# Kernel tuning notes

Hardware: AMD Instinct MI355X
Metric: run time of the kernel (lower is better)

Reference implementation:

```python
import jax, jax.numpy as jnp
import numpy as np

SDF_W = 7000.0
EIK_W = 600.0
ORI_W = 500.0
NEAR_ORI_W = 10.0
GRADN_W = 200.0
K_NEIGHBORS = 2


def _orientation_sign(query, surface, normals, k=K_NEIGHBORS):
    # Original detaches to numpy for a scipy KDTree query -> stop_gradient here.
    q = jax.lax.stop_gradient(query)       # [Q,3]
    s = jax.lax.stop_gradient(surface)     # [S,3]
    n = jax.lax.stop_gradient(normals)     # [S,3]
    # Brute-force squared distances [Q,S] (GEMM-dominated).
    d2 = (jnp.sum(q * q, axis=-1, keepdims=True)
          - 2.0 * (q @ s.T)
          + jnp.sum(s * s, axis=-1)[None, :])
    _, idx = jax.lax.top_k(-d2, k)         # [Q,k] nearest-neighbor indices
    near_pts = s[idx]                      # [Q,k,3]
    near_nrm = n[idx]                      # [Q,k,3]
    vecs = q[:, None, :] - near_pts        # [Q,k,3]
    dots = jnp.sum(vecs * near_nrm, axis=-1)  # [Q,k]
    return jnp.sign(jnp.mean(dots, axis=1))   # [Q]


def setup_inputs() -> dict:
    key = jax.random.key(0)
    ks = jax.random.split(key, 8)
    N = 16384
    return {
        "manifold_pred": jax.random.normal(ks[0], (N, 1), jnp.float32) * 0.1,
        "manifold_grad": jax.random.normal(ks[1], (N, 3), jnp.float32),
        "nonmanifold_pred": jax.random.normal(ks[2], (N, 1), jnp.float32),
        "near_points_pred": jax.random.normal(ks[3], (N, 1), jnp.float32) * 0.1,
        "surface_points": jax.random.normal(ks[4], (N, 3), jnp.float32),
        "surface_normals": jax.random.normal(ks[5], (N, 3), jnp.float32),
        "off_surface_points": jax.random.normal(ks[6], (N, 3), jnp.float32) * 1.5,
        "near_points": jax.random.normal(ks[7], (N, 3), jnp.float32),
    }


def reference(manifold_pred, manifold_grad, nonmanifold_pred, near_points_pred,
              surface_points, surface_normals, off_surface_points, near_points):
    sdf_loss = jnp.mean(manifold_pred ** 2)
    eikonal_loss = jnp.mean((jnp.linalg.norm(manifold_grad, axis=-1) - 1.0) ** 2)

    signs_off = _orientation_sign(off_surface_points, surface_points, surface_normals)
    orientation_loss = jnp.mean(jax.nn.relu(-nonmanifold_pred * signs_off[:, None]))

    signs_near = _orientation_sign(near_points, surface_points, surface_normals)
    near_surface_orientation_loss = jnp.mean(jax.nn.relu(-near_points_pred * signs_near[:, None]))

    gradient_normal_loss = jnp.mean((manifold_grad - surface_normals) ** 2)

    total = (SDF_W * sdf_loss + EIK_W * eikonal_loss + ORI_W * orientation_loss
             + NEAR_ORI_W * near_surface_orientation_loss + GRADN_W * gradient_normal_loss)
    return (total, sdf_loss, eikonal_loss, orientation_loss,
            near_surface_orientation_loss, gradient_normal_loss)
```

## Files before the change

kernel.cpp:

```cpp
#include <hip/hip_runtime.h>
#include <math.h>

#define SDF_W      7000.0f
#define EIK_W      600.0f
#define ORI_W      500.0f
#define NEAR_ORI_W 10.0f
#define GRADN_W    200.0f

#define TILE   2048
#define NWAVE  8
#define QPL    8
#define CHK    64
#define WS_STRIDE 512
#define WS_REC 4096

typedef float v2f __attribute__((ext_vector_type(2)));


__device__ __forceinline__ float nh2(float sx, float sy, float sz) {
    return -0.5f * fmaf(sx, sx, fmaf(sy, sy, sz * sz));
}
__device__ __forceinline__ float score(float qx, float qy, float qz,
                                       float sx, float sy, float sz, float nh) {
    return fmaf(qx, sx, fmaf(qy, sy, fmaf(qz, sz, nh)));
}

__global__ __launch_bounds__(512, 4) void nn_scan(
    const float* __restrict__ offq, const float* __restrict__ nearq,
    const float* __restrict__ surf,
    float* __restrict__ ws, int S, int Qoff, int QT, int splits, int segLen)
{
    __shared__ float4 tile[TILE];
    const int t    = threadIdx.x;
    const int lane = t & 63;
    const int wv   = __builtin_amdgcn_readfirstlane(t >> 6);

    const int qg = blockIdx.x / splits;
    const int sp = blockIdx.x % splits;
    const int sb = sp * segLen;
    int se = sb + segLen; if (se > S) se = S;

    float qx[QPL], qy[QPL], qz[QPL];
    #pragma unroll
    for (int k = 0; k < QPL; ++k) {
        int q = qg * 512 + k * 64 + lane;
        float x = 0.f, y = 0.f, z = 0.f;
        if (q < QT) {
            const float* p = (q < Qoff) ? (offq + 3 * q) : (nearq + 3 * (q - Qoff));
            x = p[0]; y = p[1]; z = p[2];
        }
        qx[k] = x; qy[k] = y; qz[k] = z;
    }
    v2f qx2[QPL/2], qy2[QPL/2], qz2[QPL/2];
    #pragma unroll
    for (int p = 0; p < QPL/2; ++p) {
        qx2[p] = (v2f){qx[2*p], qx[2*p+1]};
        qy2[p] = (v2f){qy[2*p], qy[2*p+1]};
        qz2[p] = (v2f){qz[2*p], qz[2*p+1]};
    }

    float M1[QPL], M2[QPL], P1[QPL], P2[QPL];
    int   c1[QPL], c2[QPL];
    const int cinit = (sb < S ? sb : 0) >> 6;
    #pragma unroll
    for (int k = 0; k < QPL; ++k) {
        M1[k] = -3.0e38f; M2[k] = -3.0e38f;
        P1[k] = -3.0e38f; P2[k] = -3.0e38f;
        c1[k] = cinit;    c2[k] = cinit;
    }

    for (int base = sb; base < se; base += TILE) {
        __syncthreads();
        #pragma unroll
        for (int k = 0; k < TILE / 512; ++k) {
            int li = k * 512 + t;
            int p  = base + li;
            float sx = 0.f, sy = 0.f, sz = 0.f, w = -3.0e38f;
            if (p < se) {
                sx = surf[3*p]; sy = surf[3*p+1]; sz = surf[3*p+2];
                w  = nh2(sx, sy, sz);
            }
            tile[li] = make_float4(sx, sy, sz, w);
        }
        __syncthreads();
        const int lo = wv * (TILE / NWAVE);
        const float4* tp = tile + lo;
        const int cidbase = (base + lo) >> 6;
        #pragma unroll 1
        for (int c = 0; c < (TILE / NWAVE) / CHK; ++c) {
            const float4* cp = tp + c * CHK;
            #pragma unroll 8
            for (int o = 0; o < CHK; ++o) {
                float4 s4 = cp[o];
                v2f sx = (v2f){s4.x, s4.x};
                v2f sy = (v2f){s4.y, s4.y};
                v2f sz = (v2f){s4.z, s4.z};
                v2f sw = (v2f){s4.w, s4.w};
                #pragma unroll
                for (int p = 0; p < QPL/2; ++p) {
                    v2f g = __builtin_elementwise_fma(qx2[p], sx,
                            __builtin_elementwise_fma(qy2[p], sy,
                            __builtin_elementwise_fma(qz2[p], sz, sw)));
                    float ga = g[0], gb = g[1];
                    M2[2*p]   = __builtin_amdgcn_fmed3f(ga, M1[2*p], M2[2*p]);
                    M1[2*p]   = fmaxf(M1[2*p], ga);
                    M2[2*p+1] = __builtin_amdgcn_fmed3f(gb, M1[2*p+1], M2[2*p+1]);
                    M1[2*p+1] = fmaxf(M1[2*p+1], gb);
                }
            }
            const int cid = cidbase + c;
            #pragma unroll
            for (int k = 0; k < QPL; ++k) {
                c1[k] = (M1[k] != P1[k]) ? cid : c1[k];  P1[k] = M1[k];
                c2[k] = (M2[k] != P2[k]) ? cid : c2[k];  P2[k] = M2[k];
            }
        }
    }

    float4* rec = tile;
    __syncthreads();
    if (wv >= 4) {
        #pragma unroll
        for (int k = 0; k < QPL; ++k)
            rec[(wv - 4) * 512 + k * 64 + lane] =
                make_float4(M1[k], M2[k], __int_as_float(c1[k]), __int_as_float(c2[k]));
    }
    __syncthreads();
    if (wv < 4) {
        #pragma unroll
        for (int k = 0; k < QPL; ++k) {
            float4 a = rec[wv * 512 + k * 64 + lane];
            float a1 = a.x, a2 = a.y;
            int ac1 = __float_as_int(a.z), ac2 = __float_as_int(a.w);
            if (a1 > M1[k])      { M2[k] = M1[k]; c2[k] = c1[k]; M1[k] = a1; c1[k] = ac1; }
            else if (a1 > M2[k]) { M2[k] = a1; c2[k] = ac1; }
            if (a2 > M2[k])      { M2[k] = a2; c2[k] = ac2; }
        }
    }
    __syncthreads();
    if (wv == 2 || wv == 3) {
        #pragma unroll
        for (int k = 0; k < QPL; ++k)
            rec[(wv - 2) * 512 + k * 64 + lane] =
                make_float4(M1[k], M2[k], __int_as_float(c1[k]), __int_as_float(c2[k]));
    }
    __syncthreads();
    if (wv < 2) {
        #pragma unroll
        for (int k = 0; k < QPL; ++k) {
            float4 a = rec[wv * 512 + k * 64 + lane];
            float a1 = a.x, a2 = a.y;
            int ac1 = __float_as_int(a.z), ac2 = __float_as_int(a.w);
            if (a1 > M1[k])      { M2[k] = M1[k]; c2[k] = c1[k]; M1[k] = a1; c1[k] = ac1; }
            else if (a1 > M2[k]) { M2[k] = a1; c2[k] = ac1; }
            if (a2 > M2[k])      { M2[k] = a2; c2[k] = ac2; }
        }
    }
    __syncthreads();
    if (wv == 1) {
        #pragma unroll
        for (int k = 0; k < QPL; ++k)
            rec[k * 64 + lane] =
                make_float4(M1[k], M2[k], __int_as_float(c1[k]), __int_as_float(c2[k]));
    }
    __syncthreads();
    if (wv == 0) {
        #pragma unroll
        for (int k = 0; k < QPL; ++k) {
            float4 a = rec[k * 64 + lane];
            float a1 = a.x, a2 = a.y;
            int ac1 = __float_as_int(a.z), ac2 = __float_as_int(a.w);
            if (a1 > M1[k])      { M2[k] = M1[k]; c2[k] = c1[k]; M1[k] = a1; c1[k] = ac1; }
            else if (a1 > M2[k]) { M2[k] = a1; c2[k] = ac1; }
            if (a2 > M2[k])      { M2[k] = a2; c2[k] = ac2; }
            int gq = qg * 512 + k * 64 + lane;
            if (gq < QT)
                ((float4*)(ws + WS_REC))[(size_t)gq * splits + sp] =
                    make_float4(M1[k], M2[k], __int_as_float(c1[k]), __int_as_float(c2[k]));
        }
    }
}

__global__ __launch_bounds__(256) void recover_k(
    const float* __restrict__ offq, const float* __restrict__ nearq,
    const float* __restrict__ surf, const float* __restrict__ norms,
    const float* __restrict__ nmpred, const float* __restrict__ nppred,
    const float* __restrict__ mp, const float* __restrict__ mg,
    const float* __restrict__ sn,
    float* __restrict__ ws, int S, int Qoff, int QT, int N, int splits)
{
    const int t    = threadIdx.x;
    const int lane = t & 63;
    const int wv   = t >> 6;
    const int gw   = blockIdx.x * 4 + wv;
    const int NW   = gridDim.x * 4;

    float ori = 0.f, nori = 0.f;
    for (int q = gw; q < QT; q += NW) {
        const float4* recs = ((const float4*)(ws + WS_REC)) + (size_t)q * splits;
        float4 r = recs[0];
        float M1 = r.x, M2 = r.y;
        int C1 = __float_as_int(r.z), C2 = __float_as_int(r.w);
        for (int i = 1; i < splits; ++i) {
            float4 a = recs[i];
            float a1 = a.x, a2 = a.y;
            int ac1 = __float_as_int(a.z), ac2 = __float_as_int(a.w);
            if (a1 > M1)      { M2 = M1; C2 = C1; M1 = a1; C1 = ac1; }
            else if (a1 > M2) { M2 = a1; C2 = ac1; }
            if (a2 > M2)      { M2 = a2; C2 = ac2; }
        }
        const bool isNear = (q >= Qoff);
        const float* qp = isNear ? (nearq + 3 * (q - Qoff)) : (offq + 3 * q);
        const float qx = qp[0], qy = qp[1], qz = qp[2];

        int j1 = C1 * CHK + lane;
        float g1 = -3.0e38f;
        if (j1 < S) {
            float sx = surf[3*j1], sy = surf[3*j1+1], sz = surf[3*j1+2];
            g1 = score(qx, qy, qz, sx, sy, sz, nh2(sx, sy, sz));
        }
        unsigned long long mk1 = __ballot(g1 == M1);
        int I1 = mk1 ? (C1 * CHK + (int)__builtin_ctzll(mk1)) : 0;

        int j2 = C2 * CHK + lane;
        float g2 = -3.0e38f;
        if (j2 < S) {
            float sx = surf[3*j2], sy = surf[3*j2+1], sz = surf[3*j2+2];
            g2 = score(qx, qy, qz, sx, sy, sz, nh2(sx, sy, sz));
        }
        unsigned long long mk2 = __ballot(g2 == M2 && j2 != I1);
        int I2 = mk2 ? (C2 * CHK + (int)__builtin_ctzll(mk2))
                     : ((I1 == 0 && S > 1) ? 1 : 0);

        float d1 = (qx - surf[3*I1]) * norms[3*I1]
                 + (qy - surf[3*I1+1]) * norms[3*I1+1]
                 + (qz - surf[3*I1+2]) * norms[3*I1+2];
        float d2 = (qx - surf[3*I2]) * norms[3*I2]
                 + (qy - surf[3*I2+1]) * norms[3*I2+1]
                 + (qz - surf[3*I2+2]) * norms[3*I2+2];
        float ms  = d1 + d2;
        float sgn = (ms > 0.f) ? 1.f : ((ms < 0.f) ? -1.f : 0.f);
        float pred = isNear ? nppred[q - Qoff] : nmpred[q];
        float term = fmaxf(0.f, -pred * sgn);
        if (isNear) nori += term; else ori += term;
    }

    float sdf = 0.f, eik = 0.f, gn = 0.f;
    const int gid = blockIdx.x * 256 + t;
    const int GT  = gridDim.x * 256;
    for (int i = gid; i < N; i += GT) {
        float p = mp[i];
        sdf += p * p;
        float gx = mg[3*i], gy = mg[3*i+1], gz = mg[3*i+2];
        float nrm = sqrtf(fmaf(gx, gx, fmaf(gy, gy, gz * gz)));
        float d = nrm - 1.0f;
        eik += d * d;
        float nx = sn[3*i], ny = sn[3*i+1], nz = sn[3*i+2];
        float dx = gx - nx, dy = gy - ny, dz = gz - nz;
        gn += fmaf(dx, dx, fmaf(dy, dy, dz * dz));
    }

    __shared__ float red[5][256];
    red[0][t] = (lane == 0) ? ori  : 0.f;
    red[1][t] = (lane == 0) ? nori : 0.f;
    red[2][t] = sdf; red[3][t] = eik; red[4][t] = gn;
    __syncthreads();
    for (int off = 128; off > 0; off >>= 1) {
        if (t < off) {
            #pragma unroll
            for (int k = 0; k < 5; ++k) red[k][t] += red[k][t + off];
        }
        __syncthreads();
    }
    if (t == 0) {
        #pragma unroll
        for (int k = 0; k < 5; ++k) ws[k * WS_STRIDE + blockIdx.x] = red[k][0];
    }
}

__global__ __launch_bounds__(256) void final_k(
    const float* __restrict__ ws, float* __restrict__ out,
    int N, int RB, int Qoff, int Qnear)
{
    __shared__ float r[5][256];
    int t = threadIdx.x;
    float s[5] = {0.f, 0.f, 0.f, 0.f, 0.f};
    for (int i = t; i < RB; i += 256) {
        #pragma unroll
        for (int k = 0; k < 5; ++k) s[k] += ws[k * WS_STRIDE + i];
    }
    #pragma unroll
    for (int k = 0; k < 5; ++k) r[k][t] = s[k];
    __syncthreads();
    for (int off = 128; off > 0; off >>= 1) {
        if (t < off) {
            #pragma unroll
            for (int k = 0; k < 5; ++k) r[k][t] += r[k][t + off];
        }
        __syncthreads();
    }
    if (t == 0) {
        float orim  = r[0][0] / (float)Qoff;
        float norim = r[1][0] / (float)Qnear;
        float sdfm  = r[2][0] / (float)N;
        float eikm  = r[3][0] / (float)N;
        float gnm   = r[4][0] / (3.0f * (float)N);
        out[0] = SDF_W * sdfm + EIK_W * eikm + ORI_W * orim
               + NEAR_ORI_W * norim + GRADN_W * gnm;
        out[1] = sdfm;
        out[2] = eikm;
        out[3] = orim;
        out[4] = norim;
        out[5] = gnm;
    }
}

extern "C" void kernel_launch(void* const* d_in, const int* in_sizes, int n_in,
                              void* d_out, int out_size, void* d_ws, size_t ws_size,
                              hipStream_t stream)
{
    const float* mp    = (const float*)d_in[0];
    const float* mg    = (const float*)d_in[1];
    const float* nmp   = (const float*)d_in[2];
    const float* npp   = (const float*)d_in[3];
    const float* sp    = (const float*)d_in[4];
    const float* sn    = (const float*)d_in[5];
    const float* offp  = (const float*)d_in[6];
    const float* nearp = (const float*)d_in[7];
    float* out = (float*)d_out;

    const int N     = in_sizes[0];
    const int S     = in_sizes[4] / 3;
    const int Qoff  = in_sizes[2];
    const int Qnear = in_sizes[3];
    const int QT    = Qoff + Qnear;

    float* ws = (float*)d_ws;

    const int qgroups = (QT + 511) / 512;
    size_t need8 = (size_t)WS_REC * 4 + (size_t)QT * 8 * 16 + 1024;
    size_t need4 = (size_t)WS_REC * 4 + (size_t)QT * 4 * 16 + 1024;
    const int splits = (ws_size >= need8) ? 8 : ((ws_size >= need4) ? 4 : 2);
    const int segLen = (((S + splits - 1) / splits) + CHK - 1) / CHK * CHK;

    const int RB = 512;
    nn_scan<<<qgroups * splits, 512, 0, stream>>>(offp, nearp, sp, ws,
                                                  S, Qoff, QT, splits, segLen);
    recover_k<<<RB, 256, 0, stream>>>(offp, nearp, sp, sn, nmp, npp,
                                      mp, mg, sn, ws, S, Qoff, QT, N, splits);
    final_k<<<1, 256, 0, stream>>>(ws, out, N, RB, Qoff, Qnear);
}
```

Measured before the change: 184.8 us.

## Scalarize scan inner loop, fuse final reduction via atomics, batch recover work

The packed v2f FMA inner loop of the nearest-neighbour scan is replaced by a plain scalar FMA loop. Chunk-id tracking now keeps the second-best chunk when the old best is demoted. The final_k launch is removed: recover_k accumulates its partial sums with atomics, and the last block to finish writes the outputs. recover_k also gives each wave 8 queries, loads the normals next to the candidate points, and picks the winner's dot product with shuffles instead of separate gathers. These changes drop one kernel launch and some gather latency, but may lose packed-math throughput in the hot loop.

```diff
diff --git a/kernel.cpp b/kernel.cpp
--- a/kernel.cpp
+++ b/kernel.cpp
@@ -11,10 +11,7 @@
 #define NWAVE  8
 #define QPL    8
 #define CHK    64
-#define WS_STRIDE 512
 #define WS_REC 4096
-
-typedef float v2f __attribute__((ext_vector_type(2)));
 
 
 __device__ __forceinline__ float nh2(float sx, float sy, float sz) {
@@ -35,6 +32,8 @@
     const int lane = t & 63;
     const int wv   = __builtin_amdgcn_readfirstlane(t >> 6);
 
+    if (blockIdx.x == 0 && t < 8) ws[t] = 0.0f;
+
     const int qg = blockIdx.x / splits;
     const int sp = blockIdx.x % splits;
     const int sb = sp * segLen;
@@ -50,13 +49,6 @@
             x = p[0]; y = p[1]; z = p[2];
         }
         qx[k] = x; qy[k] = y; qz[k] = z;
-    }
-    v2f qx2[QPL/2], qy2[QPL/2], qz2[QPL/2];
-    #pragma unroll
-    for (int p = 0; p < QPL/2; ++p) {
-        qx2[p] = (v2f){qx[2*p], qx[2*p+1]};
-        qy2[p] = (v2f){qy[2*p], qy[2*p+1]};
-        qz2[p] = (v2f){qz[2*p], qz[2*p+1]};
     }
 
     float M1[QPL], M2[QPL], P1[QPL], P2[QPL];
@@ -92,87 +84,50 @@
             #pragma unroll 8
             for (int o = 0; o < CHK; ++o) {
                 float4 s4 = cp[o];
-                v2f sx = (v2f){s4.x, s4.x};
-                v2f sy = (v2f){s4.y, s4.y};
-                v2f sz = (v2f){s4.z, s4.z};
-                v2f sw = (v2f){s4.w, s4.w};
                 #pragma unroll
-                for (int p = 0; p < QPL/2; ++p) {
-                    v2f g = __builtin_elementwise_fma(qx2[p], sx,
-                            __builtin_elementwise_fma(qy2[p], sy,
-                            __builtin_elementwise_fma(qz2[p], sz, sw)));
-                    float ga = g[0], gb = g[1];
-                    M2[2*p]   = __builtin_amdgcn_fmed3f(ga, M1[2*p], M2[2*p]);
-                    M1[2*p]   = fmaxf(M1[2*p], ga);
-                    M2[2*p+1] = __builtin_amdgcn_fmed3f(gb, M1[2*p+1], M2[2*p+1]);
-                    M1[2*p+1] = fmaxf(M1[2*p+1], gb);
+                for (int k = 0; k < QPL; ++k) {
+                    float g = score(qx[k], qy[k], qz[k], s4.x, s4.y, s4.z, s4.w);
+                    M2[k] = __builtin_amdgcn_fmed3f(g, M1[k], M2[k]);
+                    M1[k] = fmaxf(M1[k], g);
                 }
             }
             const int cid = cidbase + c;
             #pragma unroll
             for (int k = 0; k < QPL; ++k) {
-                c1[k] = (M1[k] != P1[k]) ? cid : c1[k];  P1[k] = M1[k];
-                c2[k] = (M2[k] != P2[k]) ? cid : c2[k];  P2[k] = M2[k];
+                int oc1 = c1[k];
+                c2[k] = (M2[k] != P2[k]) ? ((M2[k] == P1[k]) ? oc1 : cid) : c2[k];
+                c1[k] = (M1[k] != P1[k]) ? cid : oc1;
+                P1[k] = M1[k]; P2[k] = M2[k];
             }
         }
     }
 
     float4* rec = tile;
-    __syncthreads();
-    if (wv >= 4) {
-        #pragma unroll
-        for (int k = 0; k < QPL; ++k)
-            rec[(wv - 4) * 512 + k * 64 + lane] =
-                make_float4(M1[k], M2[k], __int_as_float(c1[k]), __int_as_float(c2[k]));
-    }
-    __syncthreads();
-    if (wv < 4) {
-        #pragma unroll
-        for (int k = 0; k < QPL; ++k) {
-            float4 a = rec[wv * 512 + k * 64 + lane];
-            float a1 = a.x, a2 = a.y;
-            int ac1 = __float_as_int(a.z), ac2 = __float_as_int(a.w);
-            if (a1 > M1[k])      { M2[k] = M1[k]; c2[k] = c1[k]; M1[k] = a1; c1[k] = ac1; }
-            else if (a1 > M2[k]) { M2[k] = a1; c2[k] = ac1; }
-            if (a2 > M2[k])      { M2[k] = a2; c2[k] = ac2; }
-        }
-    }
-    __syncthreads();
-    if (wv == 2 || wv == 3) {
-        #pragma unroll
-        for (int k = 0; k < QPL; ++k)
-            rec[(wv - 2) * 512 + k * 64 + lane] =
-                make_float4(M1[k], M2[k], __int_as_float(c1[k]), __int_as_float(c2[k]));
-    }
-    __syncthreads();
-    if (wv < 2) {
-        #pragma unroll
-        for (int k = 0; k < QPL; ++k) {
-            float4 a = rec[wv * 512 + k * 64 + lane];
-            float a1 = a.x, a2 = a.y;
-            int ac1 = __float_as_int(a.z), ac2 = __float_as_int(a.w);
-            if (a1 > M1[k])      { M2[k] = M1[k]; c2[k] = c1[k]; M1[k] = a1; c1[k] = ac1; }
-            else if (a1 > M2[k]) { M2[k] = a1; c2[k] = ac1; }
-            if (a2 > M2[k])      { M2[k] = a2; c2[k] = ac2; }
-        }
-    }
-    __syncthreads();
-    if (wv == 1) {
-        #pragma unroll
-        for (int k = 0; k < QPL; ++k)
-            rec[k * 64 + lane] =
-                make_float4(M1[k], M2[k], __int_as_float(c1[k]), __int_as_float(c2[k]));
-    }
-    __syncthreads();
+    #pragma unroll
+    for (int stage = 4; stage >= 1; stage >>= 1) {
+        __syncthreads();
+        if (wv >= stage && wv < 2 * stage) {
+            #pragma unroll
+            for (int k = 0; k < QPL; ++k)
+                rec[(wv - stage) * 512 + k * 64 + lane] =
+                    make_float4(M1[k], M2[k], __int_as_float(c1[k]), __int_as_float(c2[k]));
+        }
+        __syncthreads();
+        if (wv < stage) {
+            #pragma unroll
+            for (int k = 0; k < QPL; ++k) {
+                float4 a = rec[wv * 512 + k * 64 + lane];
+                float a1 = a.x, a2 = a.y;
+                int ac1 = __float_as_int(a.z), ac2 = __float_as_int(a.w);
+                if (a1 > M1[k])      { M2[k] = M1[k]; c2[k] = c1[k]; M1[k] = a1; c1[k] = ac1; }
+                else if (a1 > M2[k]) { M2[k] = a1; c2[k] = ac1; }
+                if (a2 > M2[k])      { M2[k] = a2; c2[k] = ac2; }
+            }
+        }
+    }
     if (wv == 0) {
         #pragma unroll
         for (int k = 0; k < QPL; ++k) {
-            float4 a = rec[k * 64 + lane];
-            float a1 = a.x, a2 = a.y;
-            int ac1 = __float_as_int(a.z), ac2 = __float_as_int(a.w);
-            if (a1 > M1[k])      { M2[k] = M1[k]; c2[k] = c1[k]; M1[k] = a1; c1[k] = ac1; }
-            else if (a1 > M2[k]) { M2[k] = a1; c2[k] = ac1; }
-            if (a2 > M2[k])      { M2[k] = a2; c2[k] = ac2; }
             int gq = qg * 512 + k * 64 + lane;
             if (gq < QT)
                 ((float4*)(ws + WS_REC))[(size_t)gq * splits + sp] =
@@ -187,16 +142,19 @@
     const float* __restrict__ nmpred, const float* __restrict__ nppred,
     const float* __restrict__ mp, const float* __restrict__ mg,
     const float* __restrict__ sn,
-    float* __restrict__ ws, int S, int Qoff, int QT, int N, int splits)
+    float* __restrict__ ws, float* __restrict__ out,
+    int S, int Qoff, int QT, int N, int splits, int Qnear)
 {
     const int t    = threadIdx.x;
     const int lane = t & 63;
     const int wv   = t >> 6;
-    const int gw   = blockIdx.x * 4 + wv;
-    const int NW   = gridDim.x * 4;
 
     float ori = 0.f, nori = 0.f;
-    for (int q = gw; q < QT; q += NW) {
+    const int qbase = (blockIdx.x * 4 + wv) * 8;
+    #pragma unroll 1
+    for (int u = 0; u < 8; ++u) {
+        int q = qbase + u;
+        if (q >= QT) break;
         const float4* recs = ((const float4*)(ws + WS_REC)) + (size_t)q * splits;
         float4 r = recs[0];
         float M1 = r.x, M2 = r.y;
@@ -212,35 +170,32 @@
         const bool isNear = (q >= Qoff);
         const float* qp = isNear ? (nearq + 3 * (q - Qoff)) : (offq + 3 * q);
         const float qx = qp[0], qy = qp[1], qz = qp[2];
+        const float pred = isNear ? nppred[q - Qoff] : nmpred[q];
 
         int j1 = C1 * CHK + lane;
-        float g1 = -3.0e38f;
+        int j2 = C2 * CHK + lane;
+        float g1 = -3.0e38f, d1l = 0.f, g2 = -3.0e38f, d2l = 0.f;
         if (j1 < S) {
             float sx = surf[3*j1], sy = surf[3*j1+1], sz = surf[3*j1+2];
-            g1 = score(qx, qy, qz, sx, sy, sz, nh2(sx, sy, sz));
-        }
-        unsigned long long mk1 = __ballot(g1 == M1);
-        int I1 = mk1 ? (C1 * CHK + (int)__builtin_ctzll(mk1)) : 0;
-
-        int j2 = C2 * CHK + lane;
-        float g2 = -3.0e38f;
+            float nx = norms[3*j1], ny = norms[3*j1+1], nz = norms[3*j1+2];
+            g1  = score(qx, qy, qz, sx, sy, sz, nh2(sx, sy, sz));
+            d1l = (qx - sx) * nx + (qy - sy) * ny + (qz - sz) * nz;
+        }
         if (j2 < S) {
             float sx = surf[3*j2], sy = surf[3*j2+1], sz = surf[3*j2+2];
-            g2 = score(qx, qy, qz, sx, sy, sz, nh2(sx, sy, sz));
-        }
-        unsigned long long mk2 = __ballot(g2 == M2 && j2 != I1);
-        int I2 = mk2 ? (C2 * CHK + (int)__builtin_ctzll(mk2))
-                     : ((I1 == 0 && S > 1) ? 1 : 0);
-
-        float d1 = (qx - surf[3*I1]) * norms[3*I1]
-                 + (qy - surf[3*I1+1]) * norms[3*I1+1]
-                 + (qz - surf[3*I1+2]) * norms[3*I1+2];
-        float d2 = (qx - surf[3*I2]) * norms[3*I2]
-                 + (qy - surf[3*I2+1]) * norms[3*I2+1]
-                 + (qz - surf[3*I2+2]) * norms[3*I2+2];
+            float nx = norms[3*j2], ny = norms[3*j2+1], nz = norms[3*j2+2];
+            g2  = score(qx, qy, qz, sx, sy, sz, nh2(sx, sy, sz));
+            d2l = (qx - sx) * nx + (qy - sy) * ny + (qz - sz) * nz;
+        }
+        unsigned long long mk1 = __ballot(g1 == M1);
+        int lane1 = mk1 ? (int)__builtin_ctzll(mk1) : 0;
+        float d1 = __shfl(d1l, lane1);
+        unsigned long long mk2 = __ballot(g2 == M2);
+        if (C1 == C2 && mk1) mk2 &= ~(1ull << lane1);
+        float d2 = mk2 ? __shfl(d2l, (int)__builtin_ctzll(mk2)) : d1;
+
         float ms  = d1 + d2;
         float sgn = (ms > 0.f) ? 1.f : ((ms < 0.f) ? -1.f : 0.f);
-        float pred = isNear ? nppred[q - Qoff] : nmpred[q];
         float term = fmaxf(0.f, -pred * sgn);
         if (isNear) nori += term; else ori += term;
     }
@@ -274,44 +229,23 @@
     }
     if (t == 0) {
         #pragma unroll
-        for (int k = 0; k < 5; ++k) ws[k * WS_STRIDE + blockIdx.x] = red[k][0];
-    }
-}
-
-__global__ __launch_bounds__(256) void final_k(
-    const float* __restrict__ ws, float* __restrict__ out,
-    int N, int RB, int Qoff, int Qnear)
-{
-    __shared__ float r[5][256];
-    int t = threadIdx.x;
-    float s[5] = {0.f, 0.f, 0.f, 0.f, 0.f};
-    for (int i = t; i < RB; i += 256) {
-        #pragma unroll
-        for (int k = 0; k < 5; ++k) s[k] += ws[k * WS_STRIDE + i];
-    }
-    #pragma unroll
-    for (int k = 0; k < 5; ++k) r[k][t] = s[k];
-    __syncthreads();
-    for (int off = 128; off > 0; off >>= 1) {
-        if (t < off) {
-            #pragma unroll
-            for (int k = 0; k < 5; ++k) r[k][t] += r[k][t + off];
-        }
-        __syncthreads();
-    }
-    if (t == 0) {
-        float orim  = r[0][0] / (float)Qoff;
-        float norim = r[1][0] / (float)Qnear;
-        float sdfm  = r[2][0] / (float)N;
-        float eikm  = r[3][0] / (float)N;
-        float gnm   = r[4][0] / (3.0f * (float)N);
-        out[0] = SDF_W * sdfm + EIK_W * eikm + ORI_W * orim
-               + NEAR_ORI_W * norim + GRADN_W * gnm;
-        out[1] = sdfm;
-        out[2] = eikm;
-        out[3] = orim;
-        out[4] = norim;
-        out[5] = gnm;
+        for (int k = 0; k < 5; ++k) atomicAdd(&ws[k], red[k][0]);
+        __threadfence();
+        unsigned old = atomicAdd((unsigned*)ws + 7, 1u);
+        if (old == gridDim.x - 1) {
+            float orim  = atomicAdd(&ws[0], 0.f) / (float)Qoff;
+            float norim = atomicAdd(&ws[1], 0.f) / (float)Qnear;
+            float sdfm  = atomicAdd(&ws[2], 0.f) / (float)N;
+            float eikm  = atomicAdd(&ws[3], 0.f) / (float)N;
+            float gnm   = atomicAdd(&ws[4], 0.f) / (3.0f * (float)N);
+            out[0] = SDF_W * sdfm + EIK_W * eikm + ORI_W * orim
+                   + NEAR_ORI_W * norim + GRADN_W * gnm;
+            out[1] = sdfm;
+            out[2] = eikm;
+            out[3] = orim;
+            out[4] = norim;
+            out[5] = gnm;
+        }
     }
 }
 
@@ -343,10 +277,10 @@
     const int splits = (ws_size >= need8) ? 8 : ((ws_size >= need4) ? 4 : 2);
     const int segLen = (((S + splits - 1) / splits) + CHK - 1) / CHK * CHK;
 
-    const int RB = 512;
+    const int RB = (QT + 31) / 32;
     nn_scan<<<qgroups * splits, 512, 0, stream>>>(offp, nearp, sp, ws,
                                                   S, Qoff, QT, splits, segLen);
     recover_k<<<RB, 256, 0, stream>>>(offp, nearp, sp, sn, nmp, npp,
-                                      mp, mg, sn, ws, S, Qoff, QT, N, splits);
-    final_k<<<1, 256, 0, stream>>>(ws, out, N, RB, Qoff, Qnear);
-}
+                                      mp, mg, sn, ws, out, S, Qoff, QT, N,
+                                      splits, Qnear);
+}
```

Result: slower. 233.8 us (+26.5%).
